# Performance work log

Hardware: AMD Instinct MI355X
Metric: run time of the kernel (lower is better)

## Reference

```python
import jax, jax.numpy as jnp
import numpy as np

B, T, D, EXP, K = 4, 2048, 1024, 2, 4
H = D * EXP


def setup_inputs() -> dict:
    key = jax.random.key(0)
    ks = jax.random.split(key, 8)
    x = jax.random.normal(ks[0], (B, T, D), jnp.float32)
    W_in = jax.random.normal(ks[1], (2 * H, D), jnp.float32) * D ** -0.5
    s_conv = 1.0 / np.sqrt(K)  # fan_in = (in_ch/groups)*K = K
    W_conv = jax.random.uniform(ks[2], (H, 1, K), jnp.float32, -s_conv, s_conv)
    b_conv = jax.random.uniform(ks[3], (H,), jnp.float32, -s_conv, s_conv)
    W_gates = jax.random.normal(ks[4], (3 * H, H), jnp.float32) * H ** -0.5
    s_g = 1.0 / np.sqrt(H)
    b_gates = jax.random.uniform(ks[5], (3 * H,), jnp.float32, -s_g, s_g)
    W_out = jax.random.normal(ks[6], (D, H), jnp.float32) * H ** -0.5
    alpha_p = jnp.asarray(1.0, jnp.float32)
    return {"x": x, "W_in": W_in, "W_conv": W_conv, "b_conv": b_conv,
            "W_gates": W_gates, "b_gates": b_gates, "W_out": W_out,
            "alpha_p": alpha_p}


def _scan_combine(c1, c2):
    a1, b1 = c1
    a2, b2 = c2
    return (a1 * a2, a2 * b1 + b2)


def reference(x, W_in, W_conv, b_conv, W_gates, b_gates, W_out, alpha_p):
    # input projection -> gate branch and conv branch, each [B,T,H]
    gi = jnp.einsum('btd,ed->bte', x, W_in)
    gate, u = jnp.split(gi, 2, axis=-1)
    # causal depthwise conv over time (torch pads K-1 both sides then keeps [:T])
    uc = jnp.transpose(u, (0, 2, 1))  # [B,H,T]
    v = jax.lax.conv_general_dilated(
        uc, W_conv, window_strides=(1,), padding=[(K - 1, 0)],
        dimension_numbers=('NCH', 'OIH', 'NCH'), feature_group_count=H)
    v = jnp.transpose(v + b_conv[None, :, None], (0, 2, 1))  # [B,T,H]
    # gates
    g = jnp.einsum('bth,gh->btg', v, W_gates) + b_gates
    f, i, o = jnp.split(g, 3, axis=-1)
    # reversed_sigmoid=True: alpha = sigmoid(-f) ** relu(alpha_p)
    alpha = jax.nn.sigmoid(-f) ** jax.nn.relu(alpha_p)
    xin = jax.nn.sigmoid(i) * v
    # diagonal linear recurrence h_t = alpha_t * h_{t-1} + xin_t via parallel scan
    _, h = jax.lax.associative_scan(_scan_combine, (alpha, xin), axis=1)
    h = jax.nn.sigmoid(o) * h
    return jnp.einsum('bth,dh->btd', jax.nn.gelu(gate, approximate=False) * h, W_out)
```

## Files before the change

### kernel.cpp

```cpp
#include <hip/hip_runtime.h>
#include <hip/hip_bf16.h>
#include <cstdint>
#include <cstddef>

#define B_ 4
#define T_ 2048
#define D_ 1024
#define H_ 2048

typedef __attribute__((ext_vector_type(8))) short s8v;
typedef __attribute__((ext_vector_type(4))) float f4v;

__device__ __forceinline__ float bflo(unsigned int u){ union{unsigned int i;float f;}c; c.i=u<<16; return c.f; }
__device__ __forceinline__ float bfhi(unsigned int u){ union{unsigned int i;float f;}c; c.i=u&0xffff0000u; return c.f; }
__device__ __forceinline__ unsigned short f2bf(float f){
    __hip_bfloat16 h = __float2bfloat16(f);
    union { __hip_bfloat16 h; unsigned short u; } c; c.h = h; return c.u;
}
__device__ __forceinline__ unsigned int pk2(float lo, float hi){
    return (unsigned int)f2bf(lo) | ((unsigned int)f2bf(hi) << 16);
}
__device__ __forceinline__ float sigm(float x){ return 1.f/(1.f+expf(-x)); }

__device__ __forceinline__ void gload16(const void* g, void* l){
    __builtin_amdgcn_global_load_lds(
        (const __attribute__((address_space(1))) unsigned int*)g,
        (__attribute__((address_space(3))) unsigned int*)l, 16, 0, 0);
}

__global__ __launch_bounds__(256)
void cvt8(const float* __restrict__ s, unsigned short* __restrict__ d)
{
    size_t i = ((size_t)blockIdx.x*256 + threadIdx.x)*8;
    float4 a = *(const float4*)(s+i), b = *(const float4*)(s+i+4);
    uint4 o; o.x=pk2(a.x,a.y); o.y=pk2(a.z,a.w); o.z=pk2(b.x,b.y); o.w=pk2(b.z,b.w);
    *(uint4*)(d+i)=o;
}

template<int EPI>
__global__ __launch_bounds__(512, 2)
void pgemm(const unsigned short* __restrict__ A, int lda,
           const unsigned short* __restrict__ Bw, int K, int N,
           const float* __restrict__ bias,
           unsigned short* __restrict__ C0, unsigned short* __restrict__ C1,
           unsigned short* __restrict__ C2,
           const unsigned short* __restrict__ vsrc, const float* __restrict__ app)
{
    __shared__ unsigned short lds[4][16384];
    const int tid = threadIdx.x;
    const int lane = tid & 63;
    const int wid = tid >> 6;
    const int wm = wid >> 2;
    const int wn = wid & 3;

    const int nwg = (N >> 8) * 32;
    const int orig = blockIdx.x;
    const int q = nwg >> 3;
    const int wg = (orig & 7) * q + (orig >> 3);
    const int m0 = (wg & 31) * 256;
    const int n0 = (wg >> 5) * 256;

    const char* srcA[2]; const char* srcB[2];
    int dstOff[2];
#pragma unroll
    for (int r = 0; r < 2; ++r) {
        int si = r*512 + tid;
        int rp = si >> 3;
        int sl = (si & 7) ^ (rp & 7);
        int row = 2*rp + (sl >> 2);
        int fg  = sl & 3;
        srcA[r] = (const char*)(A  + (size_t)(m0 + row) * lda + fg*8);
        srcB[r] = (const char*)(Bw + (size_t)(n0 + row) * K   + fg*8);
        dstOff[r] = (r*512 + wid*64) * 16;
    }

    const int fr = lane & 15, fg = lane >> 4;
    int aoff[8], boff[4];
#pragma unroll
    for (int m = 0; m < 8; ++m) {
        int row = wm*128 + m*16 + fr;
        int rp = row >> 1;
        int sl = ((row & 1)*4 + fg) ^ (rp & 7);
        aoff[m] = rp*128 + sl*16;
    }
#pragma unroll
    for (int n = 0; n < 4; ++n) {
        int row = wn*64 + n*16 + fr;
        int rp = row >> 1;
        int sl = ((row & 1)*4 + fg) ^ (rp & 7);
        boff[n] = 16384 + rp*128 + sl*16;
    }

    f4v acc[8][4];
#pragma unroll
    for (int m = 0; m < 8; ++m)
#pragma unroll
        for (int n = 0; n < 4; ++n) { f4v z4 = {0.f,0.f,0.f,0.f}; acc[m][n] = z4; }

    const int NT = K >> 5;
    auto stage = [&](int t) {
        char* base = (char*)&lds[t & 3][0];
        const size_t ko = (size_t)t * 64;
#pragma unroll
        for (int r = 0; r < 2; ++r) gload16(srcA[r] + ko, base + dstOff[r]);
#pragma unroll
        for (int r = 0; r < 2; ++r) gload16(srcB[r] + ko, base + 16384 + dstOff[r]);
    };

    stage(0); stage(1); stage(2);
    asm volatile("s_waitcnt vmcnt(8)" ::: "memory");
    __builtin_amdgcn_s_barrier();
    __builtin_amdgcn_sched_barrier(0);

    for (int t = 0; t < NT; ++t) {
        const char* buf = (const char*)&lds[t & 3][0];
        if (t + 3 < NT) stage(t + 3);
        s8v a[8], b[4];
#pragma unroll
        for (int m = 0; m < 8; ++m) a[m] = *(const s8v*)(buf + aoff[m]);
#pragma unroll
        for (int n = 0; n < 4; ++n) b[n] = *(const s8v*)(buf + boff[n]);
        __builtin_amdgcn_s_setprio(1);
#pragma unroll
        for (int m = 0; m < 8; ++m)
#pragma unroll
            for (int n = 0; n < 4; ++n)
                acc[m][n] = __builtin_amdgcn_mfma_f32_16x16x32_bf16(a[m], b[n], acc[m][n], 0, 0, 0);
        __builtin_amdgcn_s_setprio(0);
        if (t + 3 < NT)       { asm volatile("s_waitcnt vmcnt(8)" ::: "memory"); }
        else if (t + 3 == NT) { asm volatile("s_waitcnt vmcnt(4)" ::: "memory"); }
        else if (t + 2 == NT) { asm volatile("s_waitcnt vmcnt(0)" ::: "memory"); }
        if (t + 1 < NT) {
            __builtin_amdgcn_s_barrier();
            __builtin_amdgcn_sched_barrier(0);
        }
    }

    float apv = 1.f; bool ap1 = true;
    if (EPI == 2) { apv = fmaxf(app[0], 0.f); ap1 = (apv == 1.0f); }
    const int cr = (lane >> 4) * 4;
    const int cc = lane & 15;
#pragma unroll
    for (int m = 0; m < 8; ++m) {
        const int grow0 = m0 + wm*128 + m*16 + cr;
#pragma unroll
        for (int n = 0; n < 4; ++n) {
            const int colb = n0 + wn*64 + n*16;
            const int gcol = colb + cc;
            if (EPI == 1) {
                unsigned short* dst = (colb < H_) ? C0 : C1;
                const int pc = gcol & (H_-1);
#pragma unroll
                for (int j = 0; j < 4; ++j)
                    dst[(size_t)(grow0+j)*H_ + pc] = f2bf(acc[m][n][j]);
            } else {
                const int plane = colb >> 11;
                const int pc = gcol & (H_-1);
#pragma unroll
                for (int j = 0; j < 4; ++j) {
                    float val = acc[m][n][j] + bias[gcol];
                    const size_t off = (size_t)(grow0+j)*H_ + pc;
                    if (plane == 0) {
                        float s = 1.f/(1.f+expf(val));
                        C0[off] = f2bf(ap1 ? s : powf(s, apv));
                    } else if (plane == 1) {
                        C1[off] = f2bf(sigm(val) * bflo(vsrc[off]));
                    } else {
                        C2[off] = f2bf(sigm(val));
                    }
                }
            }
        }
    }
}

template<int AM, int BM, int EPI>
__global__ __launch_bounds__(256)
void mgemm(const void* __restrict__ Asrc, int lda,
           const void* __restrict__ Bsrc, int K, int N,
           const float* __restrict__ bias,
           unsigned short* __restrict__ C0, unsigned short* __restrict__ C1,
           unsigned short* __restrict__ C2, float* __restrict__ Cf,
           const unsigned short* __restrict__ vsrc, const float* __restrict__ app)
{
    __shared__ unsigned short As[128*64];
    __shared__ unsigned short Bs[128*64];
    const int tid = threadIdx.x;
    const int lane = tid & 63;
    const int wid = tid >> 6;

    const int nwg = gridDim.x * 64;
    const int orig = blockIdx.y * gridDim.x + blockIdx.x;
    const int q = nwg >> 3;
    const int wg = (orig & 7) * q + (orig >> 3);
    const int m0 = (wg & 63) * 128;
    const int n0 = (wg >> 6) * 128;

    const int ar0 = wid * 32;
    const int alr = lane >> 3;
    const int alj = lane & 7;
    const int rr = tid >> 1;
    const int kh = tid & 1;

    const int wm = wid >> 1, wn = wid & 1;
    const int fr = lane & 15, fg = lane >> 4;
    int aoff[4][2], boff[4][2];
#pragma unroll
    for (int m = 0; m < 4; ++m) {
        int row = wm*64 + m*16 + fr;
#pragma unroll
        for (int s = 0; s < 2; ++s)
            aoff[m][s] = row*128 + (((s*4 + fg) ^ (row & 7)) * 16);
    }
#pragma unroll
    for (int n = 0; n < 4; ++n) {
        int row = wn*64 + n*16 + fr;
#pragma unroll
        for (int s = 0; s < 2; ++s)
            boff[n][s] = row*128 + (((s*4 + fg) ^ (row & 7)) * 16);
    }
    const char* Asc = (const char*)As;
    const char* Bsc = (const char*)Bs;

    f4v acc[4][4];
#pragma unroll
    for (int m = 0; m < 4; ++m)
#pragma unroll
        for (int n = 0; n < 4; ++n) { f4v z4 = {0.f,0.f,0.f,0.f}; acc[m][n] = z4; }

    for (int k0 = 0; k0 < K; k0 += 64) {
        if (AM == 1) {
            const unsigned short* Ab = (const unsigned short*)Asrc;
#pragma unroll
            for (int i = 0; i < 4; ++i) {
                int row = ar0 + i*8 + alr;
                int ss = alj ^ alr;
                const char* g = (const char*)(Ab + (size_t)(m0+row)*lda + k0) + ss*16;
                gload16(g, (void*)((char*)As + (ar0 + i*8)*128));
            }
        } else {
            const float* src = (const float*)Asrc + (size_t)(m0+rr)*lda + k0 + kh*32;
            float4 v[8];
#pragma unroll
            for (int i = 0; i < 8; ++i) v[i] = ((const float4*)src)[i];
#pragma unroll
            for (int qd = 0; qd < 4; ++qd) {
                uint4 w;
                w.x = pk2(v[2*qd].x, v[2*qd].y);   w.y = pk2(v[2*qd].z, v[2*qd].w);
                w.z = pk2(v[2*qd+1].x, v[2*qd+1].y); w.w = pk2(v[2*qd+1].z, v[2*qd+1].w);
                int j = (kh*4 + qd) ^ (rr & 7);
                *(uint4*)((char*)As + rr*128 + j*16) = w;
            }
        }
        if (BM == 1) {
            const unsigned short* Bb = (const unsigned short*)Bsrc;
#pragma unroll
            for (int i = 0; i < 4; ++i) {
                int row = ar0 + i*8 + alr;
                int ss = alj ^ alr;
                const char* g = (const char*)(Bb + (size_t)(n0+row)*K + k0) + ss*16;
                gload16(g, (void*)((char*)Bs + (ar0 + i*8)*128));
            }
        } else {
            const float* src = (const float*)Bsrc + (size_t)(n0+rr)*K + k0 + kh*32;
            float4 v[8];
#pragma unroll
            for (int i = 0; i < 8; ++i) v[i] = ((const float4*)src)[i];
#pragma unroll
            for (int qd = 0; qd < 4; ++qd) {
                uint4 w;
                w.x = pk2(v[2*qd].x, v[2*qd].y);   w.y = pk2(v[2*qd].z, v[2*qd].w);
                w.z = pk2(v[2*qd+1].x, v[2*qd+1].y); w.w = pk2(v[2*qd+1].z, v[2*qd+1].w);
                int j = (kh*4 + qd) ^ (rr & 7);
                *(uint4*)((char*)Bs + rr*128 + j*16) = w;
            }
        }
        __syncthreads();
#pragma unroll
        for (int s = 0; s < 2; ++s) {
            s8v a[4], b[4];
#pragma unroll
            for (int m = 0; m < 4; ++m) a[m] = *(const s8v*)(Asc + aoff[m][s]);
#pragma unroll
            for (int n = 0; n < 4; ++n) b[n] = *(const s8v*)(Bsc + boff[n][s]);
#pragma unroll
            for (int m = 0; m < 4; ++m)
#pragma unroll
                for (int n = 0; n < 4; ++n)
                    acc[m][n] = __builtin_amdgcn_mfma_f32_16x16x32_bf16(a[m], b[n], acc[m][n], 0, 0, 0);
        }
        __syncthreads();
    }

    float apv = 1.f; bool ap1 = true;
    if (EPI == 2) { apv = fmaxf(app[0], 0.f); ap1 = (apv == 1.0f); }
    const int cr = (lane >> 4) * 4;
    const int cc = lane & 15;
#pragma unroll
    for (int m = 0; m < 4; ++m) {
        const int grow0 = m0 + wm*64 + m*16 + cr;
#pragma unroll
        for (int n = 0; n < 4; ++n) {
            const int colb = n0 + wn*64 + n*16;
            const int gcol = colb + cc;
            if (EPI == 0) {
#pragma unroll
                for (int j = 0; j < 4; ++j)
                    Cf[(size_t)(grow0+j)*N + gcol] = acc[m][n][j];
            } else if (EPI == 1) {
                unsigned short* dst = (colb < H_) ? C0 : C1;
                const int pc = gcol & (H_-1);
#pragma unroll
                for (int j = 0; j < 4; ++j)
                    dst[(size_t)(grow0+j)*H_ + pc] = f2bf(acc[m][n][j]);
            } else {
                const int plane = colb >> 11;
                const int pc = gcol & (H_-1);
#pragma unroll
                for (int j = 0; j < 4; ++j) {
                    float val = acc[m][n][j] + bias[gcol];
                    const size_t off = (size_t)(grow0+j)*H_ + pc;
                    if (plane == 0) {
                        float s = 1.f/(1.f+expf(val));
                        C0[off] = f2bf(ap1 ? s : powf(s, apv));
                    } else if (plane == 1) {
                        C1[off] = f2bf(sigm(val) * bflo(vsrc[off]));
                    } else {
                        C2[off] = f2bf(sigm(val));
                    }
                }
            }
        }
    }
}

__global__ __launch_bounds__(256)
void conv8(const unsigned short* __restrict__ u, const float* __restrict__ Wc,
           const float* __restrict__ bc, unsigned short* __restrict__ v)
{
    size_t i8 = ((size_t)blockIdx.x*256 + threadIdx.x) * 8;
    int h = (int)(i8 % H_);
    size_t bt = i8 / H_;
    int t = (int)(bt % T_);
    float w[8][4], acc[8];
#pragma unroll
    for (int j = 0; j < 8; ++j) {
        float4 wr = *(const float4*)(Wc + (h+j)*4);
        w[j][0]=wr.x; w[j][1]=wr.y; w[j][2]=wr.z; w[j][3]=wr.w;
        acc[j] = bc[h+j];
    }
    const unsigned short* up = u + bt*H_ + h;
#pragma unroll
    for (int k = 0; k < 4; ++k) {
        int dt = 3 - k;
        if (t >= dt) {
            uint4 r = *(const uint4*)(up - (size_t)dt*H_);
            float e[8] = {bflo(r.x),bfhi(r.x),bflo(r.y),bfhi(r.y),
                          bflo(r.z),bfhi(r.z),bflo(r.w),bfhi(r.w)};
#pragma unroll
            for (int j = 0; j < 8; ++j) acc[j] = fmaf(e[j], w[j][k], acc[j]);
        }
    }
    uint4 o;
    o.x = pk2(acc[0],acc[1]); o.y = pk2(acc[2],acc[3]);
    o.z = pk2(acc[4],acc[5]); o.w = pk2(acc[6],acc[7]);
    *(uint4*)(v + i8) = o;
}

__global__ __launch_bounds__(256)
void scan_chunk8(const unsigned short* __restrict__ al, const unsigned short* __restrict__ xi,
                 float* __restrict__ cA, float* __restrict__ cB, int CT)
{
    int hh = threadIdx.x * 8;
    int c = blockIdx.y, b = blockIdx.z;
    size_t base = ((size_t)b*T_ + (size_t)c*CT)*H_ + hh;
    float A[8], Bv[8];
#pragma unroll
    for (int j=0;j<8;++j){ A[j]=1.f; Bv[j]=0.f; }
    for (int t = 0; t < CT; ++t) {
        uint4 wa = *(const uint4*)(al+base);
        uint4 wx = *(const uint4*)(xi+base);
        float a[8]={bflo(wa.x),bfhi(wa.x),bflo(wa.y),bfhi(wa.y),bflo(wa.z),bfhi(wa.z),bflo(wa.w),bfhi(wa.w)};
        float x[8]={bflo(wx.x),bfhi(wx.x),bflo(wx.y),bfhi(wx.y),bflo(wx.z),bfhi(wx.z),bflo(wx.w),bfhi(wx.w)};
#pragma unroll
        for (int j=0;j<8;++j){ A[j]*=a[j]; Bv[j]=fmaf(a[j],Bv[j],x[j]); }
        base += H_;
    }
    size_t ci = ((size_t)b*gridDim.y + c)*H_ + hh;
    *(float4*)(cA+ci)   = (float4){A[0],A[1],A[2],A[3]};
    *(float4*)(cA+ci+4) = (float4){A[4],A[5],A[6],A[7]};
    *(float4*)(cB+ci)   = (float4){Bv[0],Bv[1],Bv[2],Bv[3]};
    *(float4*)(cB+ci+4) = (float4){Bv[4],Bv[5],Bv[6],Bv[7]};
}

__global__ __launch_bounds__(256)
void scan_carry8(const float* __restrict__ cA, const float* __restrict__ cB,
                 float* __restrict__ cin, int NC)
{
    int gt = blockIdx.x*256 + threadIdx.x;
    int hh = (gt * 8) % H_;
    int b  = (gt * 8) / H_;
    float h[8];
#pragma unroll
    for (int j=0;j<8;++j) h[j]=0.f;
    for (int c = 0; c < NC; ++c) {
        size_t ci = ((size_t)b*NC + c)*H_ + hh;
        *(float4*)(cin+ci)   = (float4){h[0],h[1],h[2],h[3]};
        *(float4*)(cin+ci+4) = (float4){h[4],h[5],h[6],h[7]};
        float4 a0 = *(const float4*)(cA+ci), a1 = *(const float4*)(cA+ci+4);
        float4 b0 = *(const float4*)(cB+ci), b1 = *(const float4*)(cB+ci+4);
        float a[8]={a0.x,a0.y,a0.z,a0.w,a1.x,a1.y,a1.z,a1.w};
        float x[8]={b0.x,b0.y,b0.z,b0.w,b1.x,b1.y,b1.z,b1.w};
#pragma unroll
        for (int j=0;j<8;++j) h[j] = fmaf(a[j], h[j], x[j]);
    }
}

__global__ __launch_bounds__(256)
void scan_apply8(const unsigned short* __restrict__ al, const unsigned short* __restrict__ xi,
                 const unsigned short* __restrict__ so, const unsigned short* __restrict__ ga,
                 const float* __restrict__ cin, unsigned short* __restrict__ z, int CT)
{
    int hh = threadIdx.x * 8;
    int c = blockIdx.y, b = blockIdx.z;
    size_t base = ((size_t)b*T_ + (size_t)c*CT)*H_ + hh;
    size_t ci = ((size_t)b*gridDim.y + c)*H_ + hh;
    float h[8];
    {
        float4 h0 = *(const float4*)(cin+ci), h1 = *(const float4*)(cin+ci+4);
        h[0]=h0.x; h[1]=h0.y; h[2]=h0.z; h[3]=h0.w;
        h[4]=h1.x; h[5]=h1.y; h[6]=h1.z; h[7]=h1.w;
    }
    for (int t = 0; t < CT; ++t) {
        uint4 wa = *(const uint4*)(al+base);
        uint4 wx = *(const uint4*)(xi+base);
        uint4 ws_ = *(const uint4*)(so+base);
        uint4 wg = *(const uint4*)(ga+base);
        float a[8]={bflo(wa.x),bfhi(wa.x),bflo(wa.y),bfhi(wa.y),bflo(wa.z),bfhi(wa.z),bflo(wa.w),bfhi(wa.w)};
        float x[8]={bflo(wx.x),bfhi(wx.x),bflo(wx.y),bfhi(wx.y),bflo(wx.z),bfhi(wx.z),bflo(wx.w),bfhi(wx.w)};
        float s[8]={bflo(ws_.x),bfhi(ws_.x),bflo(ws_.y),bfhi(ws_.y),bflo(ws_.z),bfhi(ws_.z),bflo(ws_.w),bfhi(ws_.w)};
        float g[8]={bflo(wg.x),bfhi(wg.x),bflo(wg.y),bfhi(wg.y),bflo(wg.z),bfhi(wg.z),bflo(wg.w),bfhi(wg.w)};
        float zo[8];
#pragma unroll
        for (int j=0;j<8;++j) {
            h[j] = fmaf(a[j], h[j], x[j]);
            float ge = 0.5f*g[j]*(1.f+erff(g[j]*0.70710678118654752f));
            zo[j] = ge * s[j] * h[j];
        }
        uint4 o;
        o.x = pk2(zo[0],zo[1]); o.y = pk2(zo[2],zo[3]);
        o.z = pk2(zo[4],zo[5]); o.w = pk2(zo[6],zo[7]);
        *(uint4*)(z + base) = o;
        base += H_;
    }
}

__global__ void zero_out(float* __restrict__ out, size_t n)
{
    for (size_t i = (size_t)blockIdx.x*256 + threadIdx.x; i < n; i += (size_t)gridDim.x*256)
        out[i] = 0.f;
}

extern "C" void kernel_launch(void* const* d_in, const int* in_sizes, int n_in,
                              void* d_out, int out_size, void* d_ws, size_t ws_size,
                              hipStream_t stream)
{
    const float* x       = (const float*)d_in[0];
    const float* W_in    = (const float*)d_in[1];
    const float* W_conv  = (const float*)d_in[2];
    const float* b_conv  = (const float*)d_in[3];
    const float* W_gates = (const float*)d_in[4];
    const float* b_gates = (const float*)d_in[5];
    const float* W_out   = (const float*)d_in[6];
    const float* alpha_p = (const float*)d_in[7];
    float* out = (float*)d_out;

    const size_t plane = (size_t)B_ * T_ * H_;
    unsigned short* gate = (unsigned short*)d_ws;
    unsigned short* u    = gate + plane;
    unsigned short* v    = u + plane;
    unsigned short* xin  = v + plane;
    unsigned short* so   = xin + plane;
    char* R = (char*)(so + plane);

    const size_t x_elems  = (size_t)B_*T_*D_;
    const size_t wg_elems = (size_t)3*H_*H_;
    const size_t wi_elems = (size_t)2*H_*D_;
    const size_t wo_elems = (size_t)D_*H_;
    const int NCF = 64;
    const size_t carry_b = 3*(size_t)B_*NCF*H_*4;
    const size_t Rneed = x_elems*2 > carry_b + wo_elems*2 ? x_elems*2 : carry_b + wo_elems*2;
    const size_t need_fast = 5*plane*2 + Rneed;

    if (ws_size >= need_fast && (size_t)out_size*4 >= (wg_elems + wi_elems)*2) {
        unsigned short* wgb  = (unsigned short*)d_out;
        unsigned short* winb = wgb + wg_elems;
        unsigned short* xb   = (unsigned short*)R;
        float* cAp  = (float*)R;
        float* cBp  = cAp + (size_t)B_*NCF*H_;
        float* cinp = cBp + (size_t)B_*NCF*H_;
        unsigned short* woutb = (unsigned short*)(cinp + (size_t)B_*NCF*H_);
        const int CT = T_ / NCF;

        cvt8<<<(unsigned)(x_elems/2048),  256, 0, stream>>>(x, xb);
        cvt8<<<(unsigned)(wi_elems/2048), 256, 0, stream>>>(W_in, winb);
        cvt8<<<(unsigned)(wg_elems/2048), 256, 0, stream>>>(W_gates, wgb);
        pgemm<1><<<dim3(512), 512, 0, stream>>>(
            xb, D_, winb, D_, 2*H_, nullptr, gate, u, nullptr, nullptr, nullptr);
        conv8<<<(unsigned)(plane/8/256), 256, 0, stream>>>(u, W_conv, b_conv, v);
        cvt8<<<(unsigned)(wo_elems/2048), 256, 0, stream>>>(W_out, woutb);
        pgemm<2><<<dim3(768), 512, 0, stream>>>(
            v, H_, wgb, H_, 3*H_, b_gates, u, xin, so, v, alpha_p);
        scan_chunk8<<<dim3(1,NCF,B_), 256, 0, stream>>>(u, xin, cAp, cBp, CT);
        scan_carry8<<<(B_*H_/8)/256, 256, 0, stream>>>(cAp, cBp, cinp, NCF);
        scan_apply8<<<dim3(1,NCF,B_), 256, 0, stream>>>(u, xin, so, gate, cinp, v, CT);
        mgemm<1,1,0><<<dim3(8,64), 256, 0, stream>>>(
            v, H_, woutb, H_, D_, nullptr, nullptr, nullptr, nullptr, out, nullptr, nullptr);
        return;
    }

    float* cAp = (float*)R;
    int NC = 64;
    if (ws_size < 5*plane*2 + 3*(size_t)B_*64*H_*4) {
        NC = 16;
        if (ws_size < 5*plane*2 + 3*(size_t)B_*16*H_*4) {
            zero_out<<<2048, 256, 0, stream>>>(out, (size_t)out_size);
            return;
        }
    }
    const int CT = T_ / NC;
    float* cBp  = cAp + (size_t)B_*NC*H_;
    float* cinp = cBp + (size_t)B_*NC*H_;

    mgemm<0,0,1><<<dim3(32,64), 256, 0, stream>>>(
        x, D_, W_in, D_, 2*H_, nullptr, gate, u, nullptr, nullptr, nullptr, nullptr);
    conv8<<<(unsigned)(plane/8/256), 256, 0, stream>>>(u, W_conv, b_conv, v);
    mgemm<1,0,2><<<dim3(48,64), 256, 0, stream>>>(
        v, H_, W_gates, H_, 3*H_, b_gates, u, xin, so, nullptr, v, alpha_p);
    scan_chunk8<<<dim3(1,NC,B_), 256, 0, stream>>>(u, xin, cAp, cBp, CT);
    scan_carry8<<<(B_*H_/8)/256, 256, 0, stream>>>(cAp, cBp, cinp, NC);
    scan_apply8<<<dim3(1,NC,B_), 256, 0, stream>>>(u, xin, so, gate, cinp, v, CT);
    mgemm<1,0,0><<<dim3(8,64), 256, 0, stream>>>(
        v, H_, W_out, H_, D_, nullptr, nullptr, nullptr, nullptr, out, nullptr, nullptr);
}
```

Baseline: 648.0 us.

## Restructure GEMM main loop into 8-wave ping-pong with K=64 tiles

```diff
diff --git a/kernel.cpp b/kernel.cpp
--- a/kernel.cpp
+++ b/kernel.cpp
@@ -38,15 +38,15 @@
 }
 
 template<int EPI>
-__global__ __launch_bounds__(512, 2)
-void pgemm(const unsigned short* __restrict__ A, int lda,
-           const unsigned short* __restrict__ Bw, int K, int N,
-           const float* __restrict__ bias,
-           unsigned short* __restrict__ C0, unsigned short* __restrict__ C1,
-           unsigned short* __restrict__ C2,
-           const unsigned short* __restrict__ vsrc, const float* __restrict__ app)
-{
-    __shared__ unsigned short lds[4][16384];
+__global__ __launch_bounds__(512)
+void pgemm8(const unsigned short* __restrict__ A, int lda,
+            const unsigned short* __restrict__ Bw, int K, int N,
+            const float* __restrict__ bias,
+            unsigned short* __restrict__ C0, unsigned short* __restrict__ C1,
+            unsigned short* __restrict__ C2,
+            const unsigned short* __restrict__ vsrc, const float* __restrict__ app)
+{
+    __shared__ unsigned short lds[2][4][8192];
     const int tid = threadIdx.x;
     const int lane = tid & 63;
     const int wid = tid >> 6;
@@ -60,18 +60,17 @@
     const int m0 = (wg & 31) * 256;
     const int n0 = (wg >> 5) * 256;
 
-    const char* srcA[2]; const char* srcB[2];
-    int dstOff[2];
+    const char* sA[2]; const char* sB[2]; int dOff[2];
 #pragma unroll
     for (int r = 0; r < 2; ++r) {
         int si = r*512 + tid;
         int rp = si >> 3;
-        int sl = (si & 7) ^ (rp & 7);
-        int row = 2*rp + (sl >> 2);
-        int fg  = sl & 3;
-        srcA[r] = (const char*)(A  + (size_t)(m0 + row) * lda + fg*8);
-        srcB[r] = (const char*)(Bw + (size_t)(n0 + row) * K   + fg*8);
-        dstOff[r] = (r*512 + wid*64) * 16;
+        int l  = (si & 7) ^ (rp & 7);
+        int row = 2*rp + (l >> 2);
+        int cs = l & 3;
+        sA[r] = (const char*)(A  + (size_t)(m0+row)*lda) + cs*16;
+        sB[r] = (const char*)(Bw + (size_t)(n0+row)*K)   + cs*16;
+        dOff[r] = (r*512 + wid*64) * 16;
     }
 
     const int fr = lane & 15, fg = lane >> 4;
@@ -80,15 +79,15 @@
     for (int m = 0; m < 8; ++m) {
         int row = wm*128 + m*16 + fr;
         int rp = row >> 1;
-        int sl = ((row & 1)*4 + fg) ^ (rp & 7);
-        aoff[m] = rp*128 + sl*16;
+        int l = ((row & 1)*4 + fg) ^ (rp & 7);
+        aoff[m] = rp*128 + l*16;
     }
 #pragma unroll
     for (int n = 0; n < 4; ++n) {
         int row = wn*64 + n*16 + fr;
         int rp = row >> 1;
-        int sl = ((row & 1)*4 + fg) ^ (rp & 7);
-        boff[n] = 16384 + rp*128 + sl*16;
+        int l = ((row & 1)*4 + fg) ^ (rp & 7);
+        boff[n] = rp*128 + l*16;
     }
 
     f4v acc[8][4];
@@ -97,44 +96,61 @@
 #pragma unroll
         for (int n = 0; n < 4; ++n) { f4v z4 = {0.f,0.f,0.f,0.f}; acc[m][n] = z4; }
 
-    const int NT = K >> 5;
-    auto stage = [&](int t) {
-        char* base = (char*)&lds[t & 3][0];
-        const size_t ko = (size_t)t * 64;
-#pragma unroll
-        for (int r = 0; r < 2; ++r) gload16(srcA[r] + ko, base + dstOff[r]);
-#pragma unroll
-        for (int r = 0; r < 2; ++r) gload16(srcB[r] + ko, base + 16384 + dstOff[r]);
+    const int NT = K >> 6;
+
+    auto stage_unit = [&](int tt, int u) {
+        const int op = u & 1, ku = u >> 1;
+        char* dst = (char*)&lds[tt & 1][op*2 + ku][0];
+        const size_t kb = (size_t)tt*128 + (size_t)ku*64;
+#pragma unroll
+        for (int r = 0; r < 2; ++r)
+            gload16((op ? sB[r] : sA[r]) + kb, dst + dOff[r]);
     };
 
-    stage(0); stage(1); stage(2);
-    asm volatile("s_waitcnt vmcnt(8)" ::: "memory");
+    stage_unit(0,0); stage_unit(0,1); stage_unit(0,2); stage_unit(0,3);
+    asm volatile("s_waitcnt vmcnt(4)" ::: "memory");
     __builtin_amdgcn_s_barrier();
     __builtin_amdgcn_sched_barrier(0);
 
-    for (int t = 0; t < NT; ++t) {
-        const char* buf = (const char*)&lds[t & 3][0];
-        if (t + 3 < NT) stage(t + 3);
-        s8v a[8], b[4];
-#pragma unroll
-        for (int m = 0; m < 8; ++m) a[m] = *(const s8v*)(buf + aoff[m]);
-#pragma unroll
-        for (int n = 0; n < 4; ++n) b[n] = *(const s8v*)(buf + boff[n]);
-        __builtin_amdgcn_s_setprio(1);
-#pragma unroll
-        for (int m = 0; m < 8; ++m)
-#pragma unroll
-            for (int n = 0; n < 4; ++n)
-                acc[m][n] = __builtin_amdgcn_mfma_f32_16x16x32_bf16(a[m], b[n], acc[m][n], 0, 0, 0);
-        __builtin_amdgcn_s_setprio(0);
-        if (t + 3 < NT)       { asm volatile("s_waitcnt vmcnt(8)" ::: "memory"); }
-        else if (t + 3 == NT) { asm volatile("s_waitcnt vmcnt(4)" ::: "memory"); }
-        else if (t + 2 == NT) { asm volatile("s_waitcnt vmcnt(0)" ::: "memory"); }
-        if (t + 1 < NT) {
+    auto tile = [&](int t, bool more) {
+        const int cur = t & 1;
+        s8v b[4];
+#pragma unroll
+        for (int ph = 0; ph < 4; ++ph) {
+            const int ks = ph >> 1, mh = ph & 1;
+            const char* abase = (const char*)&lds[cur][ks][0];
+            const char* bbase = (const char*)&lds[cur][2 + ks][0];
+            s8v a[4];
+#pragma unroll
+            for (int i = 0; i < 4; ++i) a[i] = *(const s8v*)(abase + aoff[mh*4 + i]);
+            if (mh == 0) {
+#pragma unroll
+                for (int j = 0; j < 4; ++j) b[j] = *(const s8v*)(bbase + boff[j]);
+            }
+            if (more) stage_unit(t + 1, ph);
             __builtin_amdgcn_s_barrier();
             __builtin_amdgcn_sched_barrier(0);
-        }
-    }
+            __builtin_amdgcn_s_setprio(1);
+#pragma unroll
+            for (int i = 0; i < 4; ++i)
+#pragma unroll
+                for (int j = 0; j < 4; ++j)
+                    acc[mh*4+i][j] = __builtin_amdgcn_mfma_f32_16x16x32_bf16(
+                        a[i], b[j], acc[mh*4+i][j], 0, 0, 0);
+            __builtin_amdgcn_s_setprio(0);
+            if (ph == 1) {
+                if (more) asm volatile("s_waitcnt vmcnt(4)" ::: "memory");
+                else      asm volatile("s_waitcnt vmcnt(0)" ::: "memory");
+            } else if (ph == 3) {
+                if (more) asm volatile("s_waitcnt vmcnt(4)" ::: "memory");
+            }
+            __builtin_amdgcn_s_barrier();
+            __builtin_amdgcn_sched_barrier(0);
+        }
+    };
+
+    for (int t = 0; t < NT - 1; ++t) tile(t, true);
+    tile(NT - 1, false);
 
     float apv = 1.f; bool ap1 = true;
     if (EPI == 2) { apv = fmaxf(app[0], 0.f); ap1 = (apv == 1.0f); }
@@ -505,11 +521,11 @@
         cvt8<<<(unsigned)(x_elems/2048),  256, 0, stream>>>(x, xb);
         cvt8<<<(unsigned)(wi_elems/2048), 256, 0, stream>>>(W_in, winb);
         cvt8<<<(unsigned)(wg_elems/2048), 256, 0, stream>>>(W_gates, wgb);
-        pgemm<1><<<dim3(512), 512, 0, stream>>>(
+        pgemm8<1><<<dim3(512), 512, 0, stream>>>(
             xb, D_, winb, D_, 2*H_, nullptr, gate, u, nullptr, nullptr, nullptr);
         conv8<<<(unsigned)(plane/8/256), 256, 0, stream>>>(u, W_conv, b_conv, v);
         cvt8<<<(unsigned)(wo_elems/2048), 256, 0, stream>>>(W_out, woutb);
-        pgemm<2><<<dim3(768), 512, 0, stream>>>(
+        pgemm8<2><<<dim3(768), 512, 0, stream>>>(
             v, H_, wgb, H_, 3*H_, b_gates, u, xin, so, v, alpha_p);
         scan_chunk8<<<dim3(1,NCF,B_), 256, 0, stream>>>(u, xin, cAp, cBp, CT);
         scan_carry8<<<(B_*H_/8)/256, 256, 0, stream>>>(cAp, cBp, cinp, NCF);
```

After: 647.4 us. Within noise of the previous version (-0.1%).
